# Kernel optimization log

Hardware: AMD Instinct MI355X
Metric: run time of the kernel (lower is better)

Reference implementation:

```python
import jax, jax.numpy as jnp
import numpy as np

B = 4
DIM = 512          # d_model
L = 4096           # n_tokens
D_STATE = 16
D_CONV = 4
EXPAND = 2
D_INNER = EXPAND * DIM          # 1024
DT_RANK = (DIM + 15) // 16      # ceil(dim/16) = 32
EPS = 1e-5


def setup_inputs() -> dict:
    key = jax.random.key(0)
    ks = jax.random.split(key, 8)
    s = 0.02
    A_log = jnp.log(jnp.tile(jnp.arange(1.0, D_STATE + 1.0, dtype=jnp.float32), (D_INNER, 1)))
    return {
        "x": jax.random.normal(ks[0], (B, DIM, L), jnp.float32),
        "ln_w": jnp.ones((DIM,), jnp.float32),
        "ln_b": jnp.zeros((DIM,), jnp.float32),
        "W_in": jax.random.normal(ks[1], (2 * D_INNER, DIM), jnp.float32) * s,
        "conv_w": jax.random.normal(ks[2], (D_INNER, 1, D_CONV), jnp.float32) * s,
        "conv_b": jnp.zeros((D_INNER,), jnp.float32),
        "W_xproj": jax.random.normal(ks[3], (DT_RANK + 2 * D_STATE, D_INNER), jnp.float32) * s,
        "W_dt": jax.random.normal(ks[4], (D_INNER, DT_RANK), jnp.float32) * s,
        "b_dt": jax.random.normal(ks[5], (D_INNER,), jnp.float32) * 0.1,
        "A_log": A_log,
        "D": jnp.ones((D_INNER,), jnp.float32),
        "W_out": jax.random.normal(ks[6], (DIM, D_INNER), jnp.float32) * s,
    }


def reference(x, ln_w, ln_b, W_in, conv_w, conv_b, W_xproj, W_dt, b_dt, A_log, D, W_out):
    Bsz = x.shape[0]
    # [B, d_model, L] -> [B, L, d_model]
    xt = jnp.swapaxes(x, 1, 2)
    # LayerNorm
    mu = jnp.mean(xt, axis=-1, keepdims=True)
    var = jnp.mean(jnp.square(xt - mu), axis=-1, keepdims=True)
    xn = (xt - mu) * jax.lax.rsqrt(var + EPS) * ln_w + ln_b
    # in_proj -> x, z branches
    xz = xn @ W_in.T                       # [B, L, 2*d_inner]
    xin, z = jnp.split(xz, 2, axis=-1)
    # causal depthwise conv1d (torch pads d_conv-1 both sides then truncates to L)
    xc = jnp.swapaxes(xin, 1, 2)           # [B, d_inner, L]
    xc = jax.lax.conv_general_dilated(
        xc, conv_w, window_strides=(1,), padding=[(D_CONV - 1, 0)],
        dimension_numbers=("NCH", "OIH", "NCH"), feature_group_count=D_INNER)
    xc = xc + conv_b[None, :, None]
    u = jax.nn.silu(jnp.swapaxes(xc, 1, 2))  # [B, L, d_inner]
    # input-dependent SSM parameters
    dbl = u @ W_xproj.T                    # [B, L, dt_rank + 2*d_state]
    dt = dbl[..., :DT_RANK]
    Bm = dbl[..., DT_RANK:DT_RANK + D_STATE]
    Cm = dbl[..., DT_RANK + D_STATE:]
    delta = jax.nn.softplus(dt @ W_dt.T + b_dt)  # [B, L, d_inner]
    A = -jnp.exp(A_log)                    # [d_inner, d_state]

    def step(h, inp):
        d_t, b_t, c_t, u_t = inp           # [B,di], [B,ds], [B,ds], [B,di]
        dA = jnp.exp(d_t[..., None] * A)   # [B, di, ds]
        h = dA * h + (d_t * u_t)[..., None] * b_t[:, None, :]
        y = jnp.einsum("bds,bs->bd", h, c_t)
        return h, y

    h0 = jnp.zeros((Bsz, D_INNER, D_STATE), x.dtype)
    xs = (jnp.swapaxes(delta, 0, 1), jnp.swapaxes(Bm, 0, 1),
          jnp.swapaxes(Cm, 0, 1), jnp.swapaxes(u, 0, 1))
    _, ys = jax.lax.scan(step, h0, xs)     # ys: [L, B, d_inner]
    y = jnp.swapaxes(ys, 0, 1) + u * D
    y = y * jax.nn.silu(z)
    out = y @ W_out.T                      # [B, L, d_model]
    return jnp.swapaxes(out, 1, 2)         # [B, d_model, L]
```

## Files before the change

kernel.cpp:

```cpp
#include <hip/hip_runtime.h>
#include <math.h>

#define Bsz 4
#define DIM 512
#define LEN 4096
#define DST 16
#define DIN 1024
#define NCH 64
#define CHL 64

typedef unsigned short ushort_t;
typedef unsigned int uint_t;
typedef __attribute__((ext_vector_type(8))) short short8;
typedef __attribute__((ext_vector_type(8))) unsigned short ushort8;
typedef __attribute__((ext_vector_type(8))) _Float16 half8;
typedef __attribute__((ext_vector_type(4))) float f32x4;

__device__ __forceinline__ float sigmoidf_(float x){ return 1.0f/(1.0f+__expf(-x)); }
__device__ __forceinline__ float bf2f(ushort_t u){ return __uint_as_float(((uint_t)u) << 16); }
__device__ __forceinline__ ushort_t f2bf(float f){
  uint_t x = __float_as_uint(f);
  uint_t r = (x + 0x7FFFu + ((x >> 16) & 1u)) >> 16;
  return (ushort_t)r;
}
__device__ __forceinline__ ushort_t f2h_bits(float f){
  _Float16 h = (_Float16)f;
  union { _Float16 h; ushort_t u; } v; v.h = h; return v.u;
}
__device__ __forceinline__ void gl2lds16(const void* g, void* l){
  __builtin_amdgcn_global_load_lds((const __attribute__((address_space(1))) void*)g,
                                   (__attribute__((address_space(3))) void*)l, 16, 0, 0);
}
#define POW_CHAIN(av, a1) \
  { float a2=a1*a1, a4=a2*a2, a8=a4*a4; \
    av[0]=a1; av[1]=a2; av[2]=a2*a1; av[3]=a4; \
    av[4]=a4*a1; av[5]=a4*a2; av[6]=a4*av[2]; av[7]=a8; \
    av[8]=a8*a1; av[9]=a8*a2; av[10]=a8*av[2]; av[11]=a8*a4; \
    av[12]=a8*av[4]; av[13]=a8*av[5]; av[14]=a8*av[6]; av[15]=a8*a8; }

__device__ __forceinline__ bool load_nA(const float* Alog, int d, float* nA){
  bool fast = true;
  #pragma unroll
  for(int s=0;s<DST;s++){
    float v = -__expf(Alog[d*DST+s]);
    float tgt = -(float)(s+1);
    if(fabsf(v - tgt) < 1e-4f*(float)(s+1)) v = tgt;
    else fast = false;
    nA[s] = v;
  }
  return fast;
}

__global__ __launch_bounds__(1024) void prep_k(const float* __restrict__ Win,
    const float* __restrict__ Wout, const float* __restrict__ Wxp,
    ushort_t* __restrict__ Winb, ushort_t* __restrict__ Woutb, ushort_t* __restrict__ Wxpb,
    const float* __restrict__ x, float* __restrict__ mu, float* __restrict__ rs){
  __shared__ float rsum[16][64], rsq[16][64];
  int bid = blockIdx.x;
  int tid = threadIdx.x;
  if(bid < 1600){
    int i = bid*1024 + tid;
    if(i < 1048576) Winb[i] = f2bf(Win[i]);
    else if(i < 1572864) Woutb[i-1048576] = f2bf(Wout[i-1048576]);
    else Wxpb[i-1572864] = f2bf(Wxp[i-1572864]);
    return;
  }
  int sid = bid - 1600;
  int b = sid >> 6;
  int lg = sid & 63;
  int lane = tid & 63;
  int dgrp = tid >> 6;
  int l = lg*64 + lane;
  const float* xb = x + (size_t)b*DIM*LEN + l;
  float s = 0.f, sq = 0.f;
  #pragma unroll 8
  for(int i=0;i<32;i++){
    int d = dgrp*32 + i;
    float v = xb[(size_t)d*LEN];
    s += v; sq += v*v;
  }
  rsum[dgrp][lane] = s; rsq[dgrp][lane] = sq;
  __syncthreads();
  if(tid < 64){
    float ts = 0.f, tq = 0.f;
    #pragma unroll
    for(int g=0; g<16; ++g){ ts += rsum[g][tid]; tq += rsq[g][tid]; }
    float m = ts * (1.0f/DIM);
    float var = tq * (1.0f/DIM) - m*m;
    mu[b*LEN + lg*64 + tid] = m;
    rs[b*LEN + lg*64 + tid] = rsqrtf(var + 1e-5f);
  }
}

__global__ __launch_bounds__(256) void xnt_k(const float* __restrict__ x,
    const float* __restrict__ mu, const float* __restrict__ rs,
    const float* __restrict__ lnw, const float* __restrict__ lnb, ushort_t* __restrict__ xnT){
  __shared__ ushort_t t[64][72];
  int bid = blockIdx.x;
  int lt = bid & 63;
  int dt_ = (bid >> 6) & 7;
  int b = bid >> 9;
  int l0 = lt*64, d0 = dt_*64;
  int ll = threadIdx.x & 63;
  int dq = threadIdx.x >> 6;
  float mul_ = mu[b*LEN + l0 + ll], rsl = rs[b*LEN + l0 + ll];
  const float* xb = x + (size_t)b*DIM*LEN;
  #pragma unroll
  for(int i=0;i<16;i++){
    int d = d0 + dq*16 + i;
    float v = xb[(size_t)d*LEN + l0 + ll];
    t[ll][dq*16 + i] = f2bf((v - mul_)*rsl*lnw[d] + lnb[d]);
  }
  __syncthreads();
  int lr = threadIdx.x >> 2, seg = threadIdx.x & 3;
  ushort_t* dst = &xnT[(size_t)(b*LEN + l0 + lr)*DIM + d0 + seg*16];
  #pragma unroll
  for(int k=0;k<4;k++){
    ushort4 v = *(const ushort4*)&t[lr][seg*16 + k*4];
    *(ushort4*)&dst[k*4] = v;
  }
}

__global__ __launch_bounds__(256) void gemm1_mfma(const ushort_t* __restrict__ A,
    const ushort_t* __restrict__ Bw, _Float16* __restrict__ xin, ushort_t* __restrict__ sz){
  __shared__ __align__(16) ushort_t smem[2*16384];
  int tid = threadIdx.x;
  int wave = tid >> 6, lane = tid & 63;
  int flat = blockIdx.y * 16 + blockIdx.x;
  int orig = (flat & 7) * 256 + (flat >> 3);
  int n0 = (orig & 15) * 128;
  int m0 = (orig >> 4) * 128;
  int wm = (wave >> 1) * 64, wn = (wave & 1) * 64;
  int lm = lane & 15;
  int lk = lane >> 4;
  int sx = lm & 7;
  f32x4 zero4 = {0.f,0.f,0.f,0.f};
  f32x4 acc[4][4];
  #pragma unroll
  for(int i=0;i<4;i++)
    #pragma unroll
    for(int j=0;j<4;j++) acc[i][j] = zero4;
  #pragma unroll
  for(int i=0;i<4;i++){
    int c = i*256 + tid, r = c >> 3, kc = c & 7;
    int kg = kc ^ (r & 7);
    gl2lds16(&A [(size_t)(m0 + r)*512 + kg*8], &smem[c*8]);
    gl2lds16(&Bw[(size_t)(n0 + r)*512 + kg*8], &smem[8192 + c*8]);
  }
  int cur = 0;
  for(int t=0; t<8; ++t){
    if(t < 7){
      int k0n = (t+1)*64;
      ushort_t* Ad = &smem[(cur^1)*16384];
      ushort_t* Bd = &smem[(cur^1)*16384 + 8192];
      #pragma unroll
      for(int i=0;i<4;i++){
        int c = i*256 + tid, r = c >> 3, kc = c & 7;
        int kg = kc ^ (r & 7);
        gl2lds16(&A [(size_t)(m0 + r)*512 + k0n + kg*8], &Ad[c*8]);
        gl2lds16(&Bw[(size_t)(n0 + r)*512 + k0n + kg*8], &Bd[c*8]);
      }
      asm volatile("s_waitcnt vmcnt(8)" ::: "memory");
    } else {
      asm volatile("s_waitcnt vmcnt(0)" ::: "memory");
    }
    __builtin_amdgcn_sched_barrier(0);
    __builtin_amdgcn_s_barrier();
    const ushort_t* As = &smem[cur*16384];
    const ushort_t* Bs = &smem[cur*16384 + 8192];
    #pragma unroll
    for(int kk=0; kk<64; kk+=32){
      short8 af[4], bf[4];
      int ch = ((kk >> 3) + lk) ^ sx;
      #pragma unroll
      for(int i=0;i<4;i++){
        af[i] = *(const short8*)&As[(wm + i*16 + lm)*64 + ch*8];
        bf[i] = *(const short8*)&Bs[(wn + i*16 + lm)*64 + ch*8];
      }
      #pragma unroll
      for(int i=0;i<4;i++)
        #pragma unroll
        for(int j=0;j<4;j++)
          acc[i][j] = __builtin_amdgcn_mfma_f32_16x16x32_bf16(af[i], bf[j], acc[i][j], 0, 0, 0);
    }
    __builtin_amdgcn_s_barrier();
    cur ^= 1;
  }
  ushort_t* T = smem;
  bool is_z = (n0 >= 1024);
  #pragma unroll
  for(int i=0;i<4;i++)
    #pragma unroll
    for(int j=0;j<4;j++)
      #pragma unroll
      for(int r=0;r<4;r++){
        int ml = wm + i*16 + lk*4 + r;
        int nl = wn + j*16 + lm;
        float v = acc[i][j][r];
        T[ml*136 + nl] = is_z ? f2bf(v * sigmoidf_(v)) : f2h_bits(v);
      }
  __syncthreads();
  int rr = tid >> 4, cc = (tid & 15)*8;
  #pragma unroll
  for(int p=0;p<8;p++){
    int row = p*16 + rr;
    ushort8 v = *(const ushort8*)&T[row*136 + cc];
    if(!is_z) *(ushort8*)((ushort_t*)xin + (size_t)(m0+row)*DIN + n0 + cc) = v;
    else      *(ushort8*)&sz[(size_t)(m0+row)*DIN + (n0-1024) + cc] = v;
  }
}

__global__ __launch_bounds__(256) void conv_silu_k(const _Float16* __restrict__ xin,
    const float* __restrict__ cw, const float* __restrict__ cb, ushort_t* __restrict__ u){
  int idx = blockIdx.x*256 + threadIdx.x;
  int dg = idx & 127;
  int lc = (idx >> 7) & 511;
  int b  = idx >> 16;
  int d0 = dg*8;
  int l0 = lc*8;
  float bias[8];
  #pragma unroll
  for(int k=0;k<8;k+=4){
    float4 c4 = *(const float4*)&cb[d0+k];
    bias[k]=c4.x; bias[k+1]=c4.y; bias[k+2]=c4.z; bias[k+3]=c4.w;
  }
  float w[8][4];
  #pragma unroll
  for(int k=0;k<8;k++){
    float4 c4 = *(const float4*)&cw[(d0+k)*4];
    w[k][0]=c4.x; w[k][1]=c4.y; w[k][2]=c4.z; w[k][3]=c4.w;
  }
  const _Float16* base = xin + ((size_t)b*LEN)*DIN + d0;
  ushort_t* ub = u + ((size_t)b*LEN)*DIN + d0;
  float f0[8], f1[8], f2[8];
  if(lc > 0){
    half8 h0 = *(const half8*)&base[(size_t)(l0-3)*DIN];
    half8 h1 = *(const half8*)&base[(size_t)(l0-2)*DIN];
    half8 h2 = *(const half8*)&base[(size_t)(l0-1)*DIN];
    #pragma unroll
    for(int k=0;k<8;k++){ f0[k]=(float)h0[k]; f1[k]=(float)h1[k]; f2[k]=(float)h2[k]; }
  } else {
    #pragma unroll
    for(int k=0;k<8;k++){ f0[k]=0.f; f1[k]=0.f; f2[k]=0.f; }
  }
  #pragma unroll
  for(int t=0;t<8;t++){
    half8 xv = *(const half8*)&base[(size_t)(l0+t)*DIN];
    float f3[8];
    #pragma unroll
    for(int k=0;k<8;k++) f3[k] = (float)xv[k];
    short8 o;
    #pragma unroll
    for(int k=0;k<8;k++){
      float a = bias[k] + f0[k]*w[k][0] + f1[k]*w[k][1] + f2[k]*w[k][2] + f3[k]*w[k][3];
      float v = a * sigmoidf_(a);
      o[k] = (short)f2bf(v);
    }
    *(short8*)&ub[(size_t)(l0+t)*DIN] = o;
    #pragma unroll
    for(int k=0;k<8;k++){ f0[k]=f1[k]; f1[k]=f2[k]; f2[k]=f3[k]; }
  }
}

__global__ __launch_bounds__(256) void gemm2_mfma(const ushort_t* __restrict__ A,
    const ushort_t* __restrict__ Bw, float* __restrict__ dbl){
  __shared__ __align__(16) ushort_t smem[2*8192];
  int tid = threadIdx.x;
  int wave = tid >> 6, lane = tid & 63;
  int m0 = blockIdx.x * 64;
  int wm = (wave >> 1) * 32, wn = (wave & 1) * 32;
  int lm = lane & 15;
  int lk = lane >> 4;
  int sx = lm & 7;
  f32x4 zero4 = {0.f,0.f,0.f,0.f};
  f32x4 acc[2][2];
  #pragma unroll
  for(int i=0;i<2;i++){ acc[i][0] = zero4; acc[i][1] = zero4; }
  #pragma unroll
  for(int i=0;i<2;i++){
    int c = i*256 + tid, r = c >> 3, kc = c & 7;
    int kg = kc ^ (r & 7);
    gl2lds16(&A [(size_t)(m0 + r)*1024 + kg*8], &smem[c*8]);
    gl2lds16(&Bw[(size_t)r*1024 + kg*8], &smem[4096 + c*8]);
  }
  int cur = 0;
  for(int t=0; t<16; ++t){
    if(t < 15){
      int k0n = (t+1)*64;
      ushort_t* Ad = &smem[(cur^1)*8192];
      ushort_t* Bd = &smem[(cur^1)*8192 + 4096];
      #pragma unroll
      for(int i=0;i<2;i++){
        int c = i*256 + tid, r = c >> 3, kc = c & 7;
        int kg = kc ^ (r & 7);
        gl2lds16(&A [(size_t)(m0 + r)*1024 + k0n + kg*8], &Ad[c*8]);
        gl2lds16(&Bw[(size_t)r*1024 + k0n + kg*8], &Bd[c*8]);
      }
      asm volatile("s_waitcnt vmcnt(4)" ::: "memory");
    } else {
      asm volatile("s_waitcnt vmcnt(0)" ::: "memory");
    }
    __builtin_amdgcn_sched_barrier(0);
    __builtin_amdgcn_s_barrier();
    const ushort_t* As = &smem[cur*8192];
    const ushort_t* Bs = &smem[cur*8192 + 4096];
    #pragma unroll
    for(int kk=0; kk<64; kk+=32){
      short8 af[2], bf[2];
      int ch = ((kk >> 3) + lk) ^ sx;
      #pragma unroll
      for(int i=0;i<2;i++) af[i] = *(const short8*)&As[(wm + i*16 + lm)*64 + ch*8];
      #pragma unroll
      for(int j=0;j<2;j++) bf[j] = *(const short8*)&Bs[(wn + j*16 + lm)*64 + ch*8];
      #pragma unroll
      for(int i=0;i<2;i++)
        #pragma unroll
        for(int j=0;j<2;j++)
          acc[i][j] = __builtin_amdgcn_mfma_f32_16x16x32_bf16(af[i], bf[j], acc[i][j], 0, 0, 0);
    }
    __builtin_amdgcn_s_barrier();
    cur ^= 1;
  }
  #pragma unroll
  for(int i=0;i<2;i++)
    #pragma unroll
    for(int j=0;j<2;j++)
      #pragma unroll
      for(int r=0;r<4;r++){
        int m = m0 + wm + i*16 + lk*4 + r;
        int n = wn + j*16 + lm;
        dbl[(size_t)m*64 + n] = acc[i][j][r];
      }
}

__global__ __launch_bounds__(256,4) void deltag_k(const float* __restrict__ dbl,
    const float* __restrict__ Wdt, const float* __restrict__ bdt,
    _Float16* __restrict__ dF){
  __shared__ __align__(16) float dts[64*32];
  int bid = blockIdx.x;
  int d0 = (bid & 3) * 256;
  int m0 = (bid >> 2) * 64;
  int tid = threadIdx.x;
  const f32x4* src4 = (const f32x4*)(dbl + (size_t)m0*64);
  f32x4* dst4 = (f32x4*)dts;
  for(int i=tid; i<64*8; i+=256){
    int row = i >> 3, q = i & 7;
    dst4[i] = src4[row*16 + q];
  }
  int d = d0 + tid;
  float w[32];
  #pragma unroll
  for(int k=0;k<32;k+=4){
    float4 t4 = *(const float4*)&Wdt[d*32+k];
    w[k]=t4.x; w[k+1]=t4.y; w[k+2]=t4.z; w[k+3]=t4.w;
  }
  float bd = bdt[d];
  __syncthreads();
  for(int m=0;m<64;m++){
    const float* row = dts + m*32;
    float dtv = bd;
    #pragma unroll
    for(int k=0;k<32;k+=4){
      f32x4 q = *(const f32x4*)&row[k];
      dtv += q.x*w[k] + q.y*w[k+1] + q.z*w[k+2] + q.w*w[k+3];
    }
    float dv = dtv > 15.f ? dtv : __logf(1.f + __expf(dtv));
    dF[(size_t)(m0+m)*DIN + d] = (_Float16)dv;
  }
}

__global__ __launch_bounds__(256,4) void scanA_k(const ushort_t* __restrict__ u,
    const float* __restrict__ dbl, const float* __restrict__ Alog,
    const _Float16* __restrict__ dF,
    float* __restrict__ E, float* __restrict__ cum){
  __shared__ __align__(16) float dch[CHL*16];
  int bid = blockIdx.x;
  int c = bid & (NCH-1);
  int dblk = (bid >> 6) & 3;
  int b = bid >> 8;
  int d = dblk*256 + threadIdx.x;
  const f32x4* src = (const f32x4*)(dbl + ((size_t)b*LEN + c*CHL)*64);
  f32x4* dst4 = (f32x4*)dch;
  for(int i=threadIdx.x; i<CHL*4; i+=256){
    int t = i >> 2, q = i & 3;
    dst4[i] = src[t*16 + 8 + q];
  }
  float nA[DST];
  bool fast = load_nA(Alog, d, nA);
  float Es[DST];
  #pragma unroll
  for(int s=0;s<DST;s++) Es[s] = 0.f;
  float cumD = 0.f;
  __syncthreads();
  const ushort_t*  uu = u  + ((size_t)b*LEN + c*CHL)*DIN + d;
  const _Float16*  pd = dF + ((size_t)b*LEN + c*CHL)*DIN + d;
  if(fast){
    for(int t=0;t<CHL;++t){
      float dv = (float)pd[(size_t)t*DIN];
      float uv = bf2f(uu[(size_t)t*DIN]);
      float du = dv*uv;
      cumD += dv;
      float a1 = __expf(-dv);
      float av[DST];
      POW_CHAIN(av, a1);
      const f32x4* r4 = (const f32x4*)(dch + t*16);
      f32x4 B0=r4[0], B1=r4[1], B2=r4[2], B3=r4[3];
      Es[0]=av[0]*Es[0]+du*B0.x;  Es[1]=av[1]*Es[1]+du*B0.y;
      Es[2]=av[2]*Es[2]+du*B0.z;  Es[3]=av[3]*Es[3]+du*B0.w;
      Es[4]=av[4]*Es[4]+du*B1.x;  Es[5]=av[5]*Es[5]+du*B1.y;
      Es[6]=av[6]*Es[6]+du*B1.z;  Es[7]=av[7]*Es[7]+du*B1.w;
      Es[8]=av[8]*Es[8]+du*B2.x;  Es[9]=av[9]*Es[9]+du*B2.y;
      Es[10]=av[10]*Es[10]+du*B2.z; Es[11]=av[11]*Es[11]+du*B2.w;
      Es[12]=av[12]*Es[12]+du*B3.x; Es[13]=av[13]*Es[13]+du*B3.y;
      Es[14]=av[14]*Es[14]+du*B3.z; Es[15]=av[15]*Es[15]+du*B3.w;
    }
  } else {
    for(int t=0;t<CHL;++t){
      float dv = (float)pd[(size_t)t*DIN];
      float uv = bf2f(uu[(size_t)t*DIN]);
      float du = dv*uv;
      cumD += dv;
      const float* row = dch + t*16;
      #pragma unroll
      for(int s=0;s<DST;s++){
        float a = __expf(dv*nA[s]);
        Es[s] = a*Es[s] + du*row[s];
      }
    }
  }
  size_t o = (size_t)(b*NCH + c)*DST*DIN + d;
  #pragma unroll
  for(int s=0;s<DST;s++) E[o + (size_t)s*DIN] = Es[s];
  cum[(size_t)(b*NCH + c)*DIN + d] = cumD;
}

__global__ __launch_bounds__(256) void scanB_k(const float* __restrict__ cum,
    const float* __restrict__ Alog, float* __restrict__ E){
  int g = blockIdx.x*256 + threadIdx.x;
  int d = g & 1023;
  int s = (g >> 10) & 15;
  int b = g >> 14;
  float v = -__expf(Alog[d*DST + s]);
  float tgt = -(float)(s+1);
  float nA = (fabsf(v - tgt) < 1e-4f*(float)(s+1)) ? tgt : v;
  float h = 0.f;
  for(int c=0;c<NCH;c++){
    float p = __expf(cum[(size_t)(b*NCH + c)*DIN + d] * nA);
    size_t o = (size_t)((b*NCH + c)*DST + s)*DIN + d;
    float e = E[o];
    E[o] = h;
    h = p*h + e;
  }
}

__global__ __launch_bounds__(256,4) void scanC_k(ushort_t* __restrict__ u,
    const float* __restrict__ dbl, const float* __restrict__ Alog,
    const float* __restrict__ Hs, const float* __restrict__ Dp, const ushort_t* __restrict__ sz,
    const _Float16* __restrict__ dF){
  __shared__ __align__(16) float dch[CHL*32];
  int bid = blockIdx.x;
  int c = bid & (NCH-1);
  int dblk = (bid >> 6) & 3;
  int b = bid >> 8;
  int d = dblk*256 + threadIdx.x;
  const f32x4* src = (const f32x4*)(dbl + ((size_t)b*LEN + c*CHL)*64);
  f32x4* dst4 = (f32x4*)dch;
  for(int i=threadIdx.x; i<CHL*8; i+=256){
    int t = i >> 3, q = i & 7;
    dst4[i] = src[t*16 + 8 + q];
  }
  float nA[DST];
  bool fast = load_nA(Alog, d, nA);
  float h[DST];
  size_t ho = (size_t)(b*NCH + c)*DST*DIN + d;
  #pragma unroll
  for(int s=0;s<DST;s++) h[s] = Hs[ho + (size_t)s*DIN];
  float Dv = Dp[d];
  __syncthreads();
  ushort_t* uu = u + ((size_t)b*LEN + c*CHL)*DIN + d;
  const ushort_t* zz = sz + ((size_t)b*LEN + c*CHL)*DIN + d;
  const _Float16* pd = dF + ((size_t)b*LEN + c*CHL)*DIN + d;
  if(fast){
    for(int t=0;t<CHL;++t){
      float dv = (float)pd[(size_t)t*DIN];
      float uv = bf2f(uu[(size_t)t*DIN]);
      float du = dv*uv;
      float a1 = __expf(-dv);
      float av[DST];
      POW_CHAIN(av, a1);
      const f32x4* r4 = (const f32x4*)(dch + t*32);
      f32x4 B0=r4[0], B1=r4[1], B2=r4[2], B3=r4[3];
      f32x4 C0=r4[4], C1=r4[5], C2=r4[6], C3=r4[7];
      float y0, y1, y2, y3;
      h[0]=av[0]*h[0]+du*B0.x;  h[1]=av[1]*h[1]+du*B0.y;
      h[2]=av[2]*h[2]+du*B0.z;  h[3]=av[3]*h[3]+du*B0.w;
      y0 = h[0]*C0.x + h[1]*C0.y; y1 = h[2]*C0.z + h[3]*C0.w;
      h[4]=av[4]*h[4]+du*B1.x;  h[5]=av[5]*h[5]+du*B1.y;
      h[6]=av[6]*h[6]+du*B1.z;  h[7]=av[7]*h[7]+du*B1.w;
      y2 = h[4]*C1.x + h[5]*C1.y; y3 = h[6]*C1.z + h[7]*C1.w;
      h[8]=av[8]*h[8]+du*B2.x;  h[9]=av[9]*h[9]+du*B2.y;
      h[10]=av[10]*h[10]+du*B2.z; h[11]=av[11]*h[11]+du*B2.w;
      y0 += h[8]*C2.x + h[9]*C2.y; y1 += h[10]*C2.z + h[11]*C2.w;
      h[12]=av[12]*h[12]+du*B3.x; h[13]=av[13]*h[13]+du*B3.y;
      h[14]=av[14]*h[14]+du*B3.z; h[15]=av[15]*h[15]+du*B3.w;
      y2 += h[12]*C3.x + h[13]*C3.y; y3 += h[14]*C3.z + h[15]*C3.w;
      float y = (y0+y1) + (y2+y3) + uv*Dv;
      y *= bf2f(zz[(size_t)t*DIN]);
      uu[(size_t)t*DIN] = f2bf(y);
    }
  } else {
    for(int t=0;t<CHL;++t){
      float dv = (float)pd[(size_t)t*DIN];
      float uv = bf2f(uu[(size_t)t*DIN]);
      float du = dv*uv;
      const float* row = dch + t*32;
      float y = 0.f;
      #pragma unroll
      for(int s=0;s<DST;s++){
        float a = __expf(dv*nA[s]);
        h[s] = a*h[s] + du*row[s];
        y += h[s]*row[16+s];
      }
      y += uv*Dv;
      y *= bf2f(zz[(size_t)t*DIN]);
      uu[(size_t)t*DIN] = f2bf(y);
    }
  }
}

__global__ __launch_bounds__(256) void gemm4_mfma(const ushort_t* __restrict__ A,
    const ushort_t* __restrict__ Bw, float* __restrict__ out){
  __shared__ __align__(16) ushort_t smem[2*16384];
  int tid = threadIdx.x;
  int wave = tid >> 6, lane = tid & 63;
  int flat = blockIdx.y * 4 + blockIdx.x;
  int orig = (flat & 7) * 64 + (flat >> 3);
  int n0 = (orig & 3) * 128;
  int m0 = (orig >> 2) * 128;
  int wm = (wave >> 1) * 64, wn = (wave & 1) * 64;
  int lm = lane & 15;
  int lk = lane >> 4;
  int sx = lm & 7;
  f32x4 zero4 = {0.f,0.f,0.f,0.f};
  f32x4 acc[4][4];
  #pragma unroll
  for(int i=0;i<4;i++)
    #pragma unroll
    for(int j=0;j<4;j++) acc[i][j] = zero4;
  #pragma unroll
  for(int i=0;i<4;i++){
    int c = i*256 + tid, r = c >> 3, kc = c & 7;
    int kg = kc ^ (r & 7);
    gl2lds16(&A [(size_t)(m0 + r)*1024 + kg*8], &smem[c*8]);
    gl2lds16(&Bw[(size_t)(n0 + r)*1024 + kg*8], &smem[8192 + c*8]);
  }
  int cur = 0;
  for(int t=0; t<16; ++t){
    if(t < 15){
      int k0n = (t+1)*64;
      ushort_t* Ad = &smem[(cur^1)*16384];
      ushort_t* Bd = &smem[(cur^1)*16384 + 8192];
      #pragma unroll
      for(int i=0;i<4;i++){
        int c = i*256 + tid, r = c >> 3, kc = c & 7;
        int kg = kc ^ (r & 7);
        gl2lds16(&A [(size_t)(m0 + r)*1024 + k0n + kg*8], &Ad[c*8]);
        gl2lds16(&Bw[(size_t)(n0 + r)*1024 + k0n + kg*8], &Bd[c*8]);
      }
      asm volatile("s_waitcnt vmcnt(8)" ::: "memory");
    } else {
      asm volatile("s_waitcnt vmcnt(0)" ::: "memory");
    }
    __builtin_amdgcn_sched_barrier(0);
    __builtin_amdgcn_s_barrier();
    const ushort_t* As = &smem[cur*16384];
    const ushort_t* Bs = &smem[cur*16384 + 8192];
    #pragma unroll
    for(int kk=0; kk<64; kk+=32){
      short8 af[4], bf[4];
      int ch = ((kk >> 3) + lk) ^ sx;
      #pragma unroll
      for(int i=0;i<4;i++){
        af[i] = *(const short8*)&As[(wm + i*16 + lm)*64 + ch*8];
        bf[i] = *(const short8*)&Bs[(wn + i*16 + lm)*64 + ch*8];
      }
      #pragma unroll
      for(int i=0;i<4;i++)
        #pragma unroll
        for(int j=0;j<4;j++)
          acc[i][j] = __builtin_amdgcn_mfma_f32_16x16x32_bf16(af[i], bf[j], acc[i][j], 0, 0, 0);
    }
    __builtin_amdgcn_s_barrier();
    cur ^= 1;
  }
  float* T = (float*)smem;
  int b = m0 >> 12, l0 = m0 & 4095;
  for(int g=0; g<4; ++g){
    __syncthreads();
    if((g >> 1) == (wave & 1)){
      int jg = g & 1;
      #pragma unroll
      for(int j2=0;j2<2;j2++){
        int j = jg*2 + j2;
        #pragma unroll
        for(int i=0;i<4;i++)
          #pragma unroll
          for(int r=0;r<4;r++){
            int ml = wm + i*16 + lk*4 + r;
            int nl = wn + j*16 + lm - g*32;
            T[nl*132 + ml] = acc[i][j][r];
          }
      }
    }
    __syncthreads();
    int nl = tid >> 3, seg = tid & 7;
    float* dst = &out[((size_t)b*DIM + n0 + g*32 + nl)*LEN + l0 + seg*16];
    #pragma unroll
    for(int k=0;k<4;k++){
      float4 v = *(const float4*)&T[nl*132 + seg*16 + k*4];
      *(float4*)&dst[k*4] = v;
    }
  }
}

extern "C" void kernel_launch(void* const* d_in, const int* in_sizes, int n_in,
                              void* d_out, int out_size, void* d_ws, size_t ws_size,
                              hipStream_t stream) {
  const float* x    = (const float*)d_in[0];
  const float* lnw  = (const float*)d_in[1];
  const float* lnb  = (const float*)d_in[2];
  const float* Win  = (const float*)d_in[3];
  const float* cw   = (const float*)d_in[4];
  const float* cb   = (const float*)d_in[5];
  const float* Wxp  = (const float*)d_in[6];
  const float* Wdt  = (const float*)d_in[7];
  const float* bdt  = (const float*)d_in[8];
  const float* Alog = (const float*)d_in[9];
  const float* Dp   = (const float*)d_in[10];
  const float* Wout = (const float*)d_in[11];
  float* out = (float*)d_out;
  float* ws  = (float*)d_ws;

  float*    mu   = ws;
  float*    rs   = ws + 16384;
  _Float16* xin  = (_Float16*)(ws + 32768);
  _Float16* dF   = (_Float16*)(ws + 32768);
  float*    E    = ws + 32768 + 8388608;
  float*    cum  = ws + 32768 + 12582912;
  ushort_t* sz   = (ushort_t*)(ws + 32768 + 16777216);
  ushort_t* u    = (ushort_t*)(ws + 32768 + 16777216 + 8388608);
  ushort_t* xnT  = (ushort_t*)(ws + 32768 + 16777216 + 16777216);
  float*    dbl  = (float*)xnT;
  ushort_t* Winb = (ushort_t*)(ws + 32768 + 16777216 + 16777216 + 4194304);
  ushort_t* Woutb= Winb + 1048576;
  ushort_t* Wxpb = Woutb + 524288;

  hipLaunchKernelGGL(prep_k,     dim3(1856),    dim3(1024), 0, stream, Win, Wout, Wxp, Winb, Woutb, Wxpb, x, mu, rs);
  hipLaunchKernelGGL(xnt_k,      dim3(2048),    dim3(256), 0, stream, x, mu, rs, lnw, lnb, xnT);
  hipLaunchKernelGGL(gemm1_mfma, dim3(16,128),  dim3(256), 0, stream, xnT, Winb, xin, sz);
  hipLaunchKernelGGL(conv_silu_k,dim3(1024),    dim3(256), 0, stream, xin, cw, cb, u);
  hipLaunchKernelGGL(gemm2_mfma, dim3(256),     dim3(256), 0, stream, u, Wxpb, dbl);
  hipLaunchKernelGGL(deltag_k,   dim3(1024),    dim3(256), 0, stream, dbl, Wdt, bdt, dF);
  hipLaunchKernelGGL(scanA_k,    dim3(1024),    dim3(256), 0, stream, u, dbl, Alog, dF, E, cum);
  hipLaunchKernelGGL(scanB_k,    dim3(256),     dim3(256), 0, stream, cum, Alog, E);
  hipLaunchKernelGGL(scanC_k,    dim3(1024),    dim3(256), 0, stream, u, dbl, Alog, E, Dp, sz, dF);
  hipLaunchKernelGGL(gemm4_mfma, dim3(4,128),   dim3(256), 0, stream, u, Woutb, out);
}
```

Before: 338.5 us.

## Restructure in_proj GEMM to 256x256 tiles with 4-stage LDS pipeline

```diff
diff --git a/kernel.cpp b/kernel.cpp
--- a/kernel.cpp
+++ b/kernel.cpp
@@ -121,92 +121,119 @@
   }
 }
 
-__global__ __launch_bounds__(256) void gemm1_mfma(const ushort_t* __restrict__ A,
+#define G1_SLOT 16384
+__global__ __launch_bounds__(512) void gemm1_mfma(const ushort_t* __restrict__ A,
     const ushort_t* __restrict__ Bw, _Float16* __restrict__ xin, ushort_t* __restrict__ sz){
-  __shared__ __align__(16) ushort_t smem[2*16384];
+  __shared__ __align__(16) ushort_t smem[4*G1_SLOT];
   int tid = threadIdx.x;
   int wave = tid >> 6, lane = tid & 63;
-  int flat = blockIdx.y * 16 + blockIdx.x;
-  int orig = (flat & 7) * 256 + (flat >> 3);
-  int n0 = (orig & 15) * 128;
-  int m0 = (orig >> 4) * 128;
-  int wm = (wave >> 1) * 64, wn = (wave & 1) * 64;
-  int lm = lane & 15;
-  int lk = lane >> 4;
-  int sx = lm & 7;
+  int flat = blockIdx.x;
+  int orig = (flat & 7) * 64 + (flat >> 3);
+  int n0 = (orig & 7) * 256;
+  int m0 = (orig >> 3) * 256;
+  int wm = wave >> 1;
+  int wn = wave & 1;
+  int lm = lane & 15, lk = lane >> 4;
   f32x4 zero4 = {0.f,0.f,0.f,0.f};
-  f32x4 acc[4][4];
+  f32x4 acc[4][8];
   #pragma unroll
   for(int i=0;i<4;i++)
     #pragma unroll
-    for(int j=0;j<4;j++) acc[i][j] = zero4;
-  #pragma unroll
-  for(int i=0;i<4;i++){
-    int c = i*256 + tid, r = c >> 3, kc = c & 7;
-    int kg = kc ^ (r & 7);
-    gl2lds16(&A [(size_t)(m0 + r)*512 + kg*8], &smem[c*8]);
-    gl2lds16(&Bw[(size_t)(n0 + r)*512 + kg*8], &smem[8192 + c*8]);
-  }
-  int cur = 0;
-  for(int t=0; t<8; ++t){
-    if(t < 7){
-      int k0n = (t+1)*64;
-      ushort_t* Ad = &smem[(cur^1)*16384];
-      ushort_t* Bd = &smem[(cur^1)*16384 + 8192];
-      #pragma unroll
-      for(int i=0;i<4;i++){
-        int c = i*256 + tid, r = c >> 3, kc = c & 7;
-        int kg = kc ^ (r & 7);
-        gl2lds16(&A [(size_t)(m0 + r)*512 + k0n + kg*8], &Ad[c*8]);
-        gl2lds16(&Bw[(size_t)(n0 + r)*512 + k0n + kg*8], &Bd[c*8]);
-      }
-      asm volatile("s_waitcnt vmcnt(8)" ::: "memory");
-    } else {
-      asm volatile("s_waitcnt vmcnt(0)" ::: "memory");
-    }
+    for(int n=0;n<8;n++) acc[i][n] = zero4;
+
+  auto STG = [&](int j, int ld){
+    int slot = j & 3;
+    int r = ld*64 + (tid >> 3);
+    int p = tid & 7;
+    int lgc = p ^ (r & 7);
+    const ushort_t* src = (lgc < 4)
+      ? &A [(size_t)(m0 + r)*512 + j*32 + lgc*8]
+      : &Bw[(size_t)(n0 + r)*512 + j*32 + (lgc-4)*8];
+    gl2lds16(src, &smem[slot*G1_SLOT + ld*4096 + tid*8]);
+  };
+
+  #pragma unroll
+  for(int jj=0; jj<3; ++jj)
+    #pragma unroll
+    for(int ld=0; ld<4; ++ld) STG(jj, ld);
+  asm volatile("s_waitcnt vmcnt(8)" ::: "memory");
+  __builtin_amdgcn_sched_barrier(0);
+  __builtin_amdgcn_s_barrier();
+
+  short8 af[4], bf[4];
+  for(int j=0; j<16; ++j){
+    const ushort_t* S = &smem[(j & 3)*G1_SLOT];
+    #pragma unroll
+    for(int i=0;i<4;i++){
+      int r = wm*64 + i*16 + lm;
+      af[i] = *(const short8*)&S[r*64 + (lk ^ (r & 7))*8];
+    }
+    #pragma unroll
+    for(int i=0;i<4;i++){
+      int r = wn*128 + i*16 + lm;
+      bf[i] = *(const short8*)&S[r*64 + (((lk+4) ^ (r & 7)))*8];
+    }
+    if(j < 13){ STG(j+3, 0); STG(j+3, 1); }
+    __builtin_amdgcn_s_barrier();
+    asm volatile("s_waitcnt lgkmcnt(0)" ::: "memory");
     __builtin_amdgcn_sched_barrier(0);
-    __builtin_amdgcn_s_barrier();
-    const ushort_t* As = &smem[cur*16384];
-    const ushort_t* Bs = &smem[cur*16384 + 8192];
-    #pragma unroll
-    for(int kk=0; kk<64; kk+=32){
-      short8 af[4], bf[4];
-      int ch = ((kk >> 3) + lk) ^ sx;
-      #pragma unroll
-      for(int i=0;i<4;i++){
-        af[i] = *(const short8*)&As[(wm + i*16 + lm)*64 + ch*8];
-        bf[i] = *(const short8*)&Bs[(wn + i*16 + lm)*64 + ch*8];
-      }
+    __builtin_amdgcn_s_setprio(1);
+    #pragma unroll
+    for(int i=0;i<4;i++)
+      #pragma unroll
+      for(int n=0;n<4;n++)
+        acc[i][n] = __builtin_amdgcn_mfma_f32_16x16x32_bf16(af[i], bf[n], acc[i][n], 0, 0, 0);
+    __builtin_amdgcn_s_setprio(0);
+    __builtin_amdgcn_s_barrier();
+    #pragma unroll
+    for(int i=0;i<4;i++){
+      int r = wn*128 + 64 + i*16 + lm;
+      bf[i] = *(const short8*)&S[r*64 + (((lk+4) ^ (r & 7)))*8];
+    }
+    if(j < 13){ STG(j+3, 2); STG(j+3, 3); }
+    __builtin_amdgcn_s_barrier();
+    asm volatile("s_waitcnt lgkmcnt(0)" ::: "memory");
+    __builtin_amdgcn_sched_barrier(0);
+    __builtin_amdgcn_s_setprio(1);
+    #pragma unroll
+    for(int i=0;i<4;i++)
+      #pragma unroll
+      for(int n=0;n<4;n++)
+        acc[i][4+n] = __builtin_amdgcn_mfma_f32_16x16x32_bf16(af[i], bf[n], acc[i][4+n], 0, 0, 0);
+    __builtin_amdgcn_s_setprio(0);
+    if(j <= 12)      asm volatile("s_waitcnt vmcnt(8)" ::: "memory");
+    else if(j == 13) asm volatile("s_waitcnt vmcnt(4)" ::: "memory");
+    else if(j == 14) asm volatile("s_waitcnt vmcnt(0)" ::: "memory");
+    __builtin_amdgcn_sched_barrier(0);
+    __builtin_amdgcn_s_barrier();
+  }
+  ushort_t* T = smem;
+  bool is_z = (n0 >= 1024);
+  for(int g=0; g<4; ++g){
+    __syncthreads();
+    if(wm == g){
       #pragma unroll
       for(int i=0;i<4;i++)
         #pragma unroll
-        for(int j=0;j<4;j++)
-          acc[i][j] = __builtin_amdgcn_mfma_f32_16x16x32_bf16(af[i], bf[j], acc[i][j], 0, 0, 0);
-    }
-    __builtin_amdgcn_s_barrier();
-    cur ^= 1;
-  }
-  ushort_t* T = smem;
-  bool is_z = (n0 >= 1024);
-  #pragma unroll
-  for(int i=0;i<4;i++)
-    #pragma unroll
-    for(int j=0;j<4;j++)
-      #pragma unroll
-      for(int r=0;r<4;r++){
-        int ml = wm + i*16 + lk*4 + r;
-        int nl = wn + j*16 + lm;
-        float v = acc[i][j][r];
-        T[ml*136 + nl] = is_z ? f2bf(v * sigmoidf_(v)) : f2h_bits(v);
-      }
-  __syncthreads();
-  int rr = tid >> 4, cc = (tid & 15)*8;
-  #pragma unroll
-  for(int p=0;p<8;p++){
-    int row = p*16 + rr;
-    ushort8 v = *(const ushort8*)&T[row*136 + cc];
-    if(!is_z) *(ushort8*)((ushort_t*)xin + (size_t)(m0+row)*DIN + n0 + cc) = v;
-    else      *(ushort8*)&sz[(size_t)(m0+row)*DIN + (n0-1024) + cc] = v;
+        for(int n=0;n<8;n++)
+          #pragma unroll
+          for(int r=0;r<4;r++){
+            int ml = i*16 + lk*4 + r;
+            int nl = wn*128 + n*16 + lm;
+            float v = acc[i][n][r];
+            T[ml*264 + nl] = is_z ? f2bf(v * sigmoidf_(v)) : f2h_bits(v);
+          }
+    }
+    __syncthreads();
+    int row = tid >> 3, cs = (tid & 7)*8;
+    #pragma unroll
+    for(int k=0;k<4;k++){
+      int col = cs + k*64;
+      ushort8 v = *(const ushort8*)&T[row*264 + col];
+      int gm = m0 + g*64 + row;
+      if(!is_z) *(ushort8*)((ushort_t*)xin + (size_t)gm*DIN + n0 + col) = v;
+      else      *(ushort8*)&sz[(size_t)gm*DIN + (n0-1024) + col] = v;
+    }
   }
 }
 
@@ -657,7 +684,7 @@
 
   hipLaunchKernelGGL(prep_k,     dim3(1856),    dim3(1024), 0, stream, Win, Wout, Wxp, Winb, Woutb, Wxpb, x, mu, rs);
   hipLaunchKernelGGL(xnt_k,      dim3(2048),    dim3(256), 0, stream, x, mu, rs, lnw, lnb, xnT);
-  hipLaunchKernelGGL(gemm1_mfma, dim3(16,128),  dim3(256), 0, stream, xnT, Winb, xin, sz);
+  hipLaunchKernelGGL(gemm1_mfma, dim3(512),     dim3(512), 0, stream, xnT, Winb, xin, sz);
   hipLaunchKernelGGL(conv_silu_k,dim3(1024),    dim3(256), 0, stream, xin, cw, cb, u);
   hipLaunchKernelGGL(gemm2_mfma, dim3(256),     dim3(256), 0, stream, u, Wxpb, dbl);
   hipLaunchKernelGGL(deltag_k,   dim3(1024),    dim3(256), 0, stream, dbl, Wdt, bdt, dF);
```

Result: slower. 346.8 us (+2.4%).
